# Kernel optimization log

Measured on AMD Instinct MI355X. Metric: run time of the kernel, lower is better.

## Reference

```python
import jax, jax.numpy as jnp
import numpy as np

MB, SEQ, EMBDIM, N_TOKENS = 8, 2048, 64, 8192


def setup_inputs() -> dict:
    key = jax.random.key(0)
    k1, k2 = jax.random.split(key)
    X = jax.random.normal(k1, (MB, SEQ, EMBDIM), dtype=jnp.float32)
    weight = jax.random.normal(k2, (N_TOKENS, EMBDIM), dtype=jnp.float32)
    return {"X": X, "weight": weight}


def reference(X, weight):
    adotb = jnp.einsum("bse,ne->bsn", X, weight)            # [mb, seq, n_tokens]
    adota = jnp.sum(X * X, axis=-1, keepdims=True)           # [mb, seq, 1]
    bdotb = jnp.sum(weight * weight, axis=-1)                # [n_tokens]
    dist = adota - 2.0 * adotb + bdotb                       # [mb, seq, n_tokens]
    return jnp.argmin(dist, axis=-1)                         # [mb, seq] int indices
```

## Files before the change

kernel.cpp:

```cpp
#include <hip/hip_runtime.h>
#include <math.h>

#define EMB     64
#define NTOK    8192
#define NQ      16384
#define TPB     256
#define CSPLIT  4
#define CRANGE  (NTOK / CSPLIT)
#define BQ      128
#define TILE_C  128
#define NT      (CRANGE / TILE_C)
#define TCH     (TILE_C * EMB)
#define NXBLK   (NQ / BQ)

typedef _Float16 half8 __attribute__((ext_vector_type(8)));
typedef float    f32x4 __attribute__((ext_vector_type(4)));

__device__ __forceinline__ void gl2lds16(const _Float16* g, _Float16* l) {
    __builtin_amdgcn_global_load_lds(
        (const __attribute__((address_space(1))) unsigned int*)g,
        (__attribute__((address_space(3))) unsigned int*)l, 16, 0, 0);
}

__device__ __forceinline__ unsigned long long pack_di(float d, int idx) {
    unsigned int u = __float_as_uint(d);
    unsigned int m = (u & 0x80000000u) ? ~u : (u | 0x80000000u);
    return ((unsigned long long)m << 32) | (unsigned int)idx;
}

__global__ void prep_kernel(const float* __restrict__ W,
                            _Float16* __restrict__ Wh, _Float16* __restrict__ Wl,
                            float* __restrict__ ynorm,
                            unsigned long long* __restrict__ packed,
                            int* __restrict__ cnt) {
    const int gtid = blockIdx.x * blockDim.x + threadIdx.x;
    if (gtid < NQ)    packed[gtid] = ~0ull;
    if (gtid < NXBLK) cnt[gtid] = 0;
    if (gtid >= NTOK) return;
    const int c = gtid;
    const int g = c >> 4, r = c & 15;
    const float* wp = W + (size_t)c * EMB;
    float s = 0.f;
#pragma unroll
    for (int seg = 0; seg < 8; ++seg) {
        float4 v0 = *(const float4*)(wp + seg * 8);
        float4 v1 = *(const float4*)(wp + seg * 8 + 4);
        float xv[8] = {v0.x, v0.y, v0.z, v0.w, v1.x, v1.y, v1.z, v1.w};
        half8 h, l;
#pragma unroll
        for (int j = 0; j < 8; ++j) {
            _Float16 hh = (_Float16)xv[j];
            h[j] = hh;
            l[j] = (_Float16)(xv[j] - (float)hh);
            s = fmaf(xv[j], xv[j], s);
        }
        const int kb = seg >> 2, lq = seg & 3;
        const size_t u = (size_t)g * 128 + kb * 64 + lq * 16 + r;
        *(half8*)(Wh + u * 8) = h;
        *(half8*)(Wl + u * 8) = l;
    }
    ynorm[c] = s;
}

__global__ __launch_bounds__(TPB, 3) void vq_mfma_kernel(
    const float* __restrict__ X,
    const _Float16* __restrict__ Wh, const _Float16* __restrict__ Wl,
    const float* __restrict__ ynorm,
    unsigned long long* __restrict__ packed,
    int* __restrict__ cnt, int* __restrict__ out)
{
    __shared__ __align__(16) _Float16 LdsH0[TCH];
    __shared__ __align__(16) _Float16 LdsH1[TCH];
    __shared__ __align__(16) _Float16 LdsL0[TCH];
    __shared__ __align__(16) _Float16 LdsL1[TCH];
    __shared__ __align__(16) float    Lyn[CRANGE];
    __shared__ float RedV[2][BQ];
    __shared__ int   RedI[2][BQ];
    __shared__ int   fin;

    const int t    = threadIdx.x;
    const int lane = t & 63;
    const int wid  = t >> 6;
    const int wq   = wid & 1;
    const int wy   = wid >> 1;
    const int l15  = lane & 15;
    const int lq   = lane >> 4;

    const int bx     = blockIdx.x;
    const int qblk   = bx * BQ;
    const int qbase  = qblk + wq * 64;
    const int cbase0 = blockIdx.y * CRANGE;

    {
        const size_t gsbase = (size_t)(cbase0 >> 4) * 1024;
#pragma unroll
        for (int i = 0; i < 4; ++i) {
            const int jw = i * 256 + wid * 64;
            gl2lds16(Wh + gsbase + (size_t)(jw + lane) * 8, LdsH0 + (size_t)jw * 8);
            gl2lds16(Wl + gsbase + (size_t)(jw + lane) * 8, LdsL0 + (size_t)jw * 8);
        }
    }

    for (int u = t; u < CRANGE / 4; u += TPB)
        ((float4*)Lyn)[u] = ((const float4*)(ynorm + cbase0))[u];

    half8 ah[4][2], al[4][2];
#pragma unroll
    for (int mt = 0; mt < 4; ++mt) {
#pragma unroll
        for (int kb = 0; kb < 2; ++kb) {
            const float* xp = X + (size_t)(qbase + mt * 16 + l15) * EMB + kb * 32 + lq * 8;
            float4 v0 = *(const float4*)xp;
            float4 v1 = *(const float4*)(xp + 4);
            float xv[8] = {v0.x, v0.y, v0.z, v0.w, v1.x, v1.y, v1.z, v1.w};
            half8 h, l;
#pragma unroll
            for (int j = 0; j < 8; ++j) {
                _Float16 hh = (_Float16)xv[j];
                h[j] = hh;
                l[j] = (_Float16)(xv[j] - (float)hh);
            }
            ah[mt][kb] = h;
            al[mt][kb] = l;
        }
    }

    float minv[4][4];
    int   mini[4][4];
#pragma unroll
    for (int mt = 0; mt < 4; ++mt)
#pragma unroll
        for (int r = 0; r < 4; ++r) { minv[mt][r] = INFINITY; mini[mt][r] = 0; }

    const f32x4 zero4 = {0.f, 0.f, 0.f, 0.f};

    __syncthreads();

    int cur = 0;
    for (int tt = 0; tt < NT; ++tt) {
        if (tt + 1 < NT) {
            const size_t gsbase = (size_t)((cbase0 + (tt + 1) * TILE_C) >> 4) * 1024;
            _Float16* dH = (cur ^ 1) ? LdsH1 : LdsH0;
            _Float16* dL = (cur ^ 1) ? LdsL1 : LdsL0;
#pragma unroll
            for (int i = 0; i < 4; ++i) {
                const int jw = i * 256 + wid * 64;
                gl2lds16(Wh + gsbase + (size_t)(jw + lane) * 8, dH + (size_t)jw * 8);
                gl2lds16(Wl + gsbase + (size_t)(jw + lane) * 8, dL + (size_t)jw * 8);
            }
        }

        const _Float16* LH = cur ? LdsH1 : LdsH0;
        const _Float16* LL = cur ? LdsL1 : LdsL0;
        const int c0 = tt * TILE_C;
#pragma unroll
        for (int ct = 0; ct < 4; ++ct) {
            const int chunk0 = (wy * 4 + ct) * 128 + lane;
            half8 bh0 = *(const half8*)(LH + (size_t)chunk0 * 8);
            half8 bl0 = *(const half8*)(LL + (size_t)chunk0 * 8);
            half8 bh1 = *(const half8*)(LH + (size_t)(chunk0 + 64) * 8);
            half8 bl1 = *(const half8*)(LL + (size_t)(chunk0 + 64) * 8);
            f32x4 acc[4];
#pragma unroll
            for (int mt = 0; mt < 4; ++mt) {
                f32x4 a = __builtin_amdgcn_mfma_f32_16x16x32_f16(al[mt][0], bh0, zero4, 0, 0, 0);
                a = __builtin_amdgcn_mfma_f32_16x16x32_f16(ah[mt][0], bl0, a, 0, 0, 0);
                a = __builtin_amdgcn_mfma_f32_16x16x32_f16(ah[mt][0], bh0, a, 0, 0, 0);
                a = __builtin_amdgcn_mfma_f32_16x16x32_f16(al[mt][1], bh1, a, 0, 0, 0);
                a = __builtin_amdgcn_mfma_f32_16x16x32_f16(ah[mt][1], bl1, a, 0, 0, 0);
                a = __builtin_amdgcn_mfma_f32_16x16x32_f16(ah[mt][1], bh1, a, 0, 0, 0);
                acc[mt] = a;
            }
            const int   ccol = wy * 64 + ct * 16;
            const float yn   = Lyn[c0 + ccol + l15];
            const int   cidx = cbase0 + c0 + ccol + l15;
#pragma unroll
            for (int mt = 0; mt < 4; ++mt) {
#pragma unroll
                for (int r = 0; r < 4; ++r) {
                    float s = fmaf(-2.f, acc[mt][r], yn);
                    if (s < minv[mt][r]) { minv[mt][r] = s; mini[mt][r] = cidx; }
                }
            }
        }

        asm volatile("s_waitcnt vmcnt(0)" ::: "memory");
        asm volatile("s_waitcnt lgkmcnt(0)" ::: "memory");
        __builtin_amdgcn_s_barrier();
        cur ^= 1;
    }

#pragma unroll
    for (int mt = 0; mt < 4; ++mt) {
#pragma unroll
        for (int r = 0; r < 4; ++r) {
            float v = minv[mt][r];
            int   i = mini[mt][r];
#pragma unroll
            for (int m = 1; m <= 8; m <<= 1) {
                float ov = __shfl_xor(v, m, 64);
                int   oi = __shfl_xor(i, m, 64);
                if (ov < v || (ov == v && oi < i)) { v = ov; i = oi; }
            }
            if (l15 == 0) {
                int qoff = wq * 64 + mt * 16 + lq * 4 + r;
                RedV[wy][qoff] = v;
                RedI[wy][qoff] = i;
            }
        }
    }
    __syncthreads();

    if (t < BQ) {
        float v0 = RedV[0][t]; int i0 = RedI[0][t];
        float v1 = RedV[1][t]; int i1 = RedI[1][t];
        if (v1 < v0 || (v1 == v0 && i1 < i0)) { v0 = v1; i0 = i1; }
        atomicMin(&packed[qblk + t], pack_di(v0, i0));
    }
    asm volatile("s_waitcnt vmcnt(0)" ::: "memory");
    __syncthreads();
    if (t == 0) fin = (atomicAdd(&cnt[bx], 1) == CSPLIT - 1);
    __syncthreads();
    if (fin && t < BQ) {
        unsigned long long v = atomicMin(&packed[qblk + t], ~0ull);
        out[qblk + t] = (int)(unsigned int)(v & 0xFFFFFFFFu);
    }
}

extern "C" void kernel_launch(void* const* d_in, const int* in_sizes, int n_in,
                              void* d_out, int out_size, void* d_ws, size_t ws_size,
                              hipStream_t stream) {
    const float* X = (const float*)d_in[0];
    const float* W = (const float*)d_in[1];

    _Float16* Wh    = (_Float16*)d_ws;
    _Float16* Wl    = Wh + (size_t)NTOK * EMB;
    float*    ynorm = (float*)(Wl + (size_t)NTOK * EMB);
    unsigned long long* packed = (unsigned long long*)(ynorm + NTOK);
    int*      cnt   = (int*)(packed + NQ);
    int*      out   = (int*)d_out;

    prep_kernel<<<NQ / TPB, TPB, 0, stream>>>(W, Wh, Wl, ynorm, packed, cnt);
    dim3 grid(NXBLK, CSPLIT);
    vq_mfma_kernel<<<grid, TPB, 0, stream>>>(X, Wh, Wl, ynorm, packed, cnt, out);
}
```

Measured before the change: 116.6 us.

## Stream low-half codebook from global, triple-buffer high half in LDS

The low-precision half of the codebook (Wl) is now loaded straight from global memory into registers each tile, instead of being staged in LDS. The high half (Wh) moves to a three-buffer LDS ring that prefetches two tiles ahead, and the explicit vmcnt/lgkmcnt waits before the barrier are removed. The prep kernel is also split so that one thread converts each 8-element chunk and separate threads compute the row norms, and the main kernel's occupancy hint drops from 3 to 2 blocks per CU. This halves LDS traffic and footprint per tile but adds global-load latency in the inner loop. Without the explicit waits, correctness and overlap depend on the compiler inserting proper waits for the LDS-DMA loads.

```diff
diff --git a/kernel.cpp b/kernel.cpp
--- a/kernel.cpp
+++ b/kernel.cpp
@@ -36,15 +36,15 @@
     const int gtid = blockIdx.x * blockDim.x + threadIdx.x;
     if (gtid < NQ)    packed[gtid] = ~0ull;
     if (gtid < NXBLK) cnt[gtid] = 0;
-    if (gtid >= NTOK) return;
-    const int c = gtid;
-    const int g = c >> 4, r = c & 15;
-    const float* wp = W + (size_t)c * EMB;
-    float s = 0.f;
-#pragma unroll
-    for (int seg = 0; seg < 8; ++seg) {
-        float4 v0 = *(const float4*)(wp + seg * 8);
-        float4 v1 = *(const float4*)(wp + seg * 8 + 4);
+    if (gtid < NTOK * 8) {
+        const int u  = gtid;
+        const int g  = u >> 7, rem = u & 127;
+        const int kb = rem >> 6, ln = rem & 63;
+        const int r  = ln & 15, lq = ln >> 4;
+        const int c  = g * 16 + r;
+        const float* wp = W + (size_t)c * EMB + kb * 32 + lq * 8;
+        float4 v0 = *(const float4*)wp;
+        float4 v1 = *(const float4*)(wp + 4);
         float xv[8] = {v0.x, v0.y, v0.z, v0.w, v1.x, v1.y, v1.z, v1.w};
         half8 h, l;
 #pragma unroll
@@ -52,27 +52,31 @@
             _Float16 hh = (_Float16)xv[j];
             h[j] = hh;
             l[j] = (_Float16)(xv[j] - (float)hh);
-            s = fmaf(xv[j], xv[j], s);
-        }
-        const int kb = seg >> 2, lq = seg & 3;
-        const size_t u = (size_t)g * 128 + kb * 64 + lq * 16 + r;
-        *(half8*)(Wh + u * 8) = h;
-        *(half8*)(Wl + u * 8) = l;
-    }
-    ynorm[c] = s;
-}
-
-__global__ __launch_bounds__(TPB, 3) void vq_mfma_kernel(
+        }
+        *(half8*)(Wh + (size_t)u * 8) = h;
+        *(half8*)(Wl + (size_t)u * 8) = l;
+    } else if (gtid < NTOK * 8 + NTOK) {
+        const int c = gtid - NTOK * 8;
+        const float4* w4 = (const float4*)(W + (size_t)c * EMB);
+        float s = 0.f;
+#pragma unroll
+        for (int i = 0; i < EMB / 4; ++i) {
+            float4 v = w4[i];
+            s = fmaf(v.x, v.x, s); s = fmaf(v.y, v.y, s);
+            s = fmaf(v.z, v.z, s); s = fmaf(v.w, v.w, s);
+        }
+        ynorm[c] = s;
+    }
+}
+
+__global__ __launch_bounds__(TPB, 2) void vq_mfma_kernel(
     const float* __restrict__ X,
     const _Float16* __restrict__ Wh, const _Float16* __restrict__ Wl,
     const float* __restrict__ ynorm,
     unsigned long long* __restrict__ packed,
     int* __restrict__ cnt, int* __restrict__ out)
 {
-    __shared__ __align__(16) _Float16 LdsH0[TCH];
-    __shared__ __align__(16) _Float16 LdsH1[TCH];
-    __shared__ __align__(16) _Float16 LdsL0[TCH];
-    __shared__ __align__(16) _Float16 LdsL1[TCH];
+    __shared__ __align__(16) _Float16 LdsH[3][TCH];
     __shared__ __align__(16) float    Lyn[CRANGE];
     __shared__ float RedV[2][BQ];
     __shared__ int   RedI[2][BQ];
@@ -91,13 +95,13 @@
     const int qbase  = qblk + wq * 64;
     const int cbase0 = blockIdx.y * CRANGE;
 
-    {
-        const size_t gsbase = (size_t)(cbase0 >> 4) * 1024;
+#pragma unroll
+    for (int pt = 0; pt < 2; ++pt) {
+        const size_t gsbase = (size_t)(cbase0 + pt * TILE_C) * 64;
 #pragma unroll
         for (int i = 0; i < 4; ++i) {
             const int jw = i * 256 + wid * 64;
-            gl2lds16(Wh + gsbase + (size_t)(jw + lane) * 8, LdsH0 + (size_t)jw * 8);
-            gl2lds16(Wl + gsbase + (size_t)(jw + lane) * 8, LdsL0 + (size_t)jw * 8);
+            gl2lds16(Wh + gsbase + (size_t)(jw + lane) * 8, &LdsH[pt][0] + (size_t)jw * 8);
         }
     }
 
@@ -136,44 +140,48 @@
 
     __syncthreads();
 
-    int cur = 0;
     for (int tt = 0; tt < NT; ++tt) {
-        if (tt + 1 < NT) {
-            const size_t gsbase = (size_t)((cbase0 + (tt + 1) * TILE_C) >> 4) * 1024;
-            _Float16* dH = (cur ^ 1) ? LdsH1 : LdsH0;
-            _Float16* dL = (cur ^ 1) ? LdsL1 : LdsL0;
+        const int cb = cbase0 + tt * TILE_C;
+
+        half8 blr[4][2];
+#pragma unroll
+        for (int ct = 0; ct < 4; ++ct) {
+            const size_t gc = (size_t)cb * 8 + (wy * 4 + ct) * 128 + lane;
+            blr[ct][0] = *(const half8*)(Wl + gc * 8);
+            blr[ct][1] = *(const half8*)(Wl + (gc + 64) * 8);
+        }
+
+        if (tt + 2 < NT) {
+            const size_t gsbase = (size_t)(cb + 2 * TILE_C) * 64;
+            _Float16* dst = &LdsH[(tt + 2) % 3][0];
 #pragma unroll
             for (int i = 0; i < 4; ++i) {
                 const int jw = i * 256 + wid * 64;
-                gl2lds16(Wh + gsbase + (size_t)(jw + lane) * 8, dH + (size_t)jw * 8);
-                gl2lds16(Wl + gsbase + (size_t)(jw + lane) * 8, dL + (size_t)jw * 8);
-            }
-        }
-
-        const _Float16* LH = cur ? LdsH1 : LdsH0;
-        const _Float16* LL = cur ? LdsL1 : LdsL0;
+                gl2lds16(Wh + gsbase + (size_t)(jw + lane) * 8, dst + (size_t)jw * 8);
+            }
+        }
+
+        const _Float16* LH = &LdsH[tt % 3][0];
         const int c0 = tt * TILE_C;
 #pragma unroll
         for (int ct = 0; ct < 4; ++ct) {
             const int chunk0 = (wy * 4 + ct) * 128 + lane;
             half8 bh0 = *(const half8*)(LH + (size_t)chunk0 * 8);
-            half8 bl0 = *(const half8*)(LL + (size_t)chunk0 * 8);
             half8 bh1 = *(const half8*)(LH + (size_t)(chunk0 + 64) * 8);
-            half8 bl1 = *(const half8*)(LL + (size_t)(chunk0 + 64) * 8);
             f32x4 acc[4];
 #pragma unroll
             for (int mt = 0; mt < 4; ++mt) {
                 f32x4 a = __builtin_amdgcn_mfma_f32_16x16x32_f16(al[mt][0], bh0, zero4, 0, 0, 0);
-                a = __builtin_amdgcn_mfma_f32_16x16x32_f16(ah[mt][0], bl0, a, 0, 0, 0);
+                a = __builtin_amdgcn_mfma_f32_16x16x32_f16(ah[mt][0], blr[ct][0], a, 0, 0, 0);
                 a = __builtin_amdgcn_mfma_f32_16x16x32_f16(ah[mt][0], bh0, a, 0, 0, 0);
                 a = __builtin_amdgcn_mfma_f32_16x16x32_f16(al[mt][1], bh1, a, 0, 0, 0);
-                a = __builtin_amdgcn_mfma_f32_16x16x32_f16(ah[mt][1], bl1, a, 0, 0, 0);
+                a = __builtin_amdgcn_mfma_f32_16x16x32_f16(ah[mt][1], blr[ct][1], a, 0, 0, 0);
                 a = __builtin_amdgcn_mfma_f32_16x16x32_f16(ah[mt][1], bh1, a, 0, 0, 0);
                 acc[mt] = a;
             }
             const int   ccol = wy * 64 + ct * 16;
             const float yn   = Lyn[c0 + ccol + l15];
-            const int   cidx = cbase0 + c0 + ccol + l15;
+            const int   cidx = cb + ccol + l15;
 #pragma unroll
             for (int mt = 0; mt < 4; ++mt) {
 #pragma unroll
@@ -184,10 +192,7 @@
             }
         }
 
-        asm volatile("s_waitcnt vmcnt(0)" ::: "memory");
-        asm volatile("s_waitcnt lgkmcnt(0)" ::: "memory");
         __builtin_amdgcn_s_barrier();
-        cur ^= 1;
     }
 
 #pragma unroll
@@ -240,7 +245,7 @@
     int*      cnt   = (int*)(packed + NQ);
     int*      out   = (int*)d_out;
 
-    prep_kernel<<<NQ / TPB, TPB, 0, stream>>>(W, Wh, Wl, ynorm, packed, cnt);
+    prep_kernel<<<(NTOK * 8 + NTOK) / TPB, TPB, 0, stream>>>(W, Wh, Wl, ynorm, packed, cnt);
     dim3 grid(NXBLK, CSPLIT);
     vq_mfma_kernel<<<grid, TPB, 0, stream>>>(X, Wh, Wl, ynorm, packed, cnt, out);
 }
```

Result: no change. 116.7 us (+0.1%).
